# Kernel tuning notes

Measured on AMD Instinct MI355X. Metric: run time of the kernel, lower is better.

## Reference

```python
import jax, jax.numpy as jnp
import numpy as np

B, T, E = 8, 2048, 1024  # batch, seq_len, emb_size (= output_emb_size)


def setup_inputs() -> dict:
    key = jax.random.key(0)
    k1, k2, k3, k4, k5, k6, k7 = jax.random.split(key, 7)
    return {
        "q": jax.random.normal(k1, (B, T, E), jnp.float32),
        "k": jax.random.normal(k2, (B, T, E), jnp.float32),
        "v": jax.random.normal(k3, (B, T, E), jnp.float32),
        "mask": jax.random.randint(k4, (T, T), 0, 2, jnp.int32),
        # nn.Linear weights, stored [out, in] as in torch; applied as x @ W.T
        "Wq": jax.random.normal(k5, (E, E), jnp.float32) / np.sqrt(E),
        "Wk": jax.random.normal(k6, (E, E), jnp.float32) / np.sqrt(E),
        "Wv": jax.random.normal(k7, (E, E), jnp.float32) / np.sqrt(E),
    }


def reference(q, k, v, mask, Wq, Wk, Wv):
    # QKV projections (bias-free Linear): x @ W.T
    query = jnp.einsum("bte,oe->bto", q, Wq)
    key_p = jnp.einsum("bse,oe->bso", k, Wk)
    value = jnp.einsum("bse,oe->bso", v, Wv)
    d = key_p.shape[-1]
    scores = jnp.einsum("bto,bso->bts", query, key_p) / np.sqrt(d).astype(jnp.float32)
    # torch.any(mask): mask is nonzero somewhere -> apply masked_fill(mask==0, -inf)
    scores = jnp.where(mask[None, :, :] == 0, -jnp.inf, scores)
    weights = jax.nn.softmax(scores, axis=-1)
    return jnp.einsum("bts,bso->bto", weights, value)
```

## Files before the change

### kernel.cpp

```cpp
#include <hip/hip_runtime.h>
#include <hip/hip_bf16.h>

typedef __attribute__((ext_vector_type(8))) short short8;
typedef __attribute__((ext_vector_type(8))) unsigned short ushortx8;
typedef __attribute__((ext_vector_type(4))) unsigned short ushortx4;
typedef __attribute__((ext_vector_type(4))) float floatx4;

#define NB 8
#define NT 2048
#define NE 1024

__device__ __forceinline__ unsigned short f2bf(float f){
  unsigned int u = __builtin_bit_cast(unsigned int, f);
  u += 0x7FFFu + ((u >> 16) & 1u);
  return (unsigned short)(u >> 16);
}
__device__ __forceinline__ float bf2f(unsigned short h){
  unsigned int u = ((unsigned int)h) << 16;
  return __builtin_bit_cast(float, u);
}

__device__ __forceinline__ void async16(void* lds, const void* g){
  __builtin_amdgcn_global_load_lds(
      (const __attribute__((address_space(1))) unsigned int*)g,
      (__attribute__((address_space(3))) unsigned int*)lds, 16, 0, 0);
}

__global__ __launch_bounds__(256) void cvt3(const float* __restrict__ a0,
                                            const float* __restrict__ a1,
                                            const float* __restrict__ a2,
                                            unsigned short* __restrict__ out,
                                            int n4_per){
  const float* src = blockIdx.y == 0 ? a0 : (blockIdx.y == 1 ? a1 : a2);
  unsigned short* dst = out + (size_t)blockIdx.y * (size_t)n4_per * 4;
  int i = blockIdx.x * 256 + threadIdx.x;
  if (i < n4_per){
    floatx4 f = ((const floatx4*)src)[i];
    ushortx4 o;
    o.x = f2bf(f.x); o.y = f2bf(f.y); o.z = f2bf(f.z); o.w = f2bf(f.w);
    *(ushortx4*)(dst + (size_t)i * 4) = o;
  }
}

__global__ __launch_bounds__(256) void pack_mask(const int* __restrict__ m,
                                                 unsigned long long* __restrict__ bits){
  int t = blockIdx.x * 256 + threadIdx.x;
  const int4* p = (const int4*)(m + (size_t)t * 64);
  unsigned long long w = 0;
  #pragma unroll
  for (int jj = 0; jj < 16; jj++){
    int4 v = p[jj];
    w |= (unsigned long long)(v.x != 0) << (jj * 4 + 0);
    w |= (unsigned long long)(v.y != 0) << (jj * 4 + 1);
    w |= (unsigned long long)(v.z != 0) << (jj * 4 + 2);
    w |= (unsigned long long)(v.w != 0) << (jj * 4 + 3);
  }
  bits[t] = w;
}

template<int EPI>
__global__ __launch_bounds__(256) void gemm_nt(
    const unsigned short* __restrict__ A, long strideA,
    const unsigned short* __restrict__ B, long strideB,
    void* __restrict__ Out, long strideOutBytes,
    const unsigned long long* __restrict__ mbits,
    int K, int gx, int gy)
{
  __shared__ __attribute__((aligned(16))) unsigned short As[128 * 64];
  __shared__ __attribute__((aligned(16))) unsigned short Bs[128 * 64];
  const int tid = threadIdx.x;
  const int lane = tid & 63, wave = tid >> 6;

  int L = blockIdx.x;
  int xcd = L & 7, t = L >> 3;
  int x = t % gx;
  int strip = xcd + ((t / gx) << 3);
  int y = strip % gy, z = strip / gy;
  const int m0 = y << 7, n0 = x << 7;
  const int Nn = gx << 7;

  const unsigned short* Az = A + (size_t)z * strideA;
  const unsigned short* Bz = B + (size_t)z * strideB;

  const char* gA[4]; const char* gB[4]; int lo[4];
  {
    int s0 = (wave << 8) + lane;
    #pragma unroll
    for (int i = 0; i < 4; i++){
      int s = s0 + (i << 6);
      int row = s >> 3;
      int c = (s & 7) ^ (row & 7);
      lo[i] = s << 4;
      gA[i] = (const char*)(Az + (size_t)(m0 + row) * K) + (c << 4);
      gB[i] = (const char*)(Bz + (size_t)(n0 + row) * K) + (c << 4);
    }
  }
  char* AsB = (char*)As;
  char* BsB = (char*)Bs;

  const int lm = lane & 15, qd = lane >> 4;
  const int wr = (wave >> 1) << 6, wc = (wave & 1) << 6;
  const int sw = lm & 7;
  const char* aB0 = AsB + (wr + lm) * 128 + ((qd ^ sw) << 4);
  const char* aB1 = AsB + (wr + lm) * 128 + (((4 + qd) ^ sw) << 4);
  const char* bB0 = BsB + (wc + lm) * 128 + ((qd ^ sw) << 4);
  const char* bB1 = BsB + (wc + lm) * 128 + (((4 + qd) ^ sw) << 4);

  floatx4 acc[4][4];
  floatx4 zero4 = {0.f, 0.f, 0.f, 0.f};
  #pragma unroll
  for (int a = 0; a < 4; a++)
    #pragma unroll
    for (int b = 0; b < 4; b++) acc[a][b] = zero4;

  for (int kk = 0; kk < K; kk += 64){
    #pragma unroll
    for (int i = 0; i < 4; i++){
      async16(AsB + lo[i], gA[i]);
      async16(BsB + lo[i], gB[i]);
      gA[i] += 128; gB[i] += 128;
    }
    __syncthreads();

    short8 a0[4], a1[4], b0[4], b1[4];
    #pragma unroll
    for (int mi = 0; mi < 4; mi++){
      a0[mi] = *(const short8*)(aB0 + mi * 2048);
      a1[mi] = *(const short8*)(aB1 + mi * 2048);
    }
    #pragma unroll
    for (int ni = 0; ni < 4; ni++){
      b0[ni] = *(const short8*)(bB0 + ni * 2048);
      b1[ni] = *(const short8*)(bB1 + ni * 2048);
    }
    #pragma unroll
    for (int mi = 0; mi < 4; mi++)
      #pragma unroll
      for (int ni = 0; ni < 4; ni++)
        acc[mi][ni] = __builtin_amdgcn_mfma_f32_16x16x32_bf16(a0[mi], b0[ni], acc[mi][ni], 0, 0, 0);
    #pragma unroll
    for (int mi = 0; mi < 4; mi++)
      #pragma unroll
      for (int ni = 0; ni < 4; ni++)
        acc[mi][ni] = __builtin_amdgcn_mfma_f32_16x16x32_bf16(a1[mi], b1[ni], acc[mi][ni], 0, 0, 0);
    __syncthreads();
  }

  char* OutZ = (char*)Out + (size_t)z * strideOutBytes;
  if constexpr (EPI == 1){
    int wcol = (n0 + wc) >> 6;
    #pragma unroll
    for (int mi = 0; mi < 4; mi++){
      #pragma unroll
      for (int i = 0; i < 4; i++){
        int row = m0 + wr + mi * 16 + qd * 4 + i;
        unsigned long long w = mbits[(size_t)row * (NT / 64) + wcol];
        unsigned short* po = (unsigned short*)OutZ + (size_t)row * Nn + n0 + wc;
        #pragma unroll
        for (int ni = 0; ni < 4; ni++){
          float vv = acc[mi][ni][i];
          float s = ((w >> (ni * 16 + lm)) & 1ull) ? vv * 0.03125f : -INFINITY;
          po[ni * 16 + lm] = f2bf(s);
        }
      }
    }
  } else {
    #pragma unroll
    for (int mi = 0; mi < 4; mi++){
      #pragma unroll
      for (int i = 0; i < 4; i++){
        int row = m0 + wr + mi * 16 + qd * 4 + i;
        #pragma unroll
        for (int ni = 0; ni < 4; ni++){
          int col = n0 + wc + ni * 16 + lm;
          float vv = acc[mi][ni][i];
          if constexpr (EPI == 0)
            ((unsigned short*)OutZ)[(size_t)row * Nn + col] = f2bf(vv);
          else
            ((float*)OutZ)[(size_t)row * Nn + col] = vv;
        }
      }
    }
  }
}

__global__ __launch_bounds__(256) void transpose_bf16(const unsigned short* __restrict__ in,
                                                      unsigned short* __restrict__ out,
                                                      int rows, int cols){
  __shared__ __attribute__((aligned(16))) unsigned short tile[64][72];
  const unsigned short* ib = in + (size_t)blockIdx.z * rows * cols;
  unsigned short* ob = out + (size_t)blockIdx.z * rows * cols;
  int r0 = blockIdx.x * 64;
  int c0 = blockIdx.y * 64;
  int tid = threadIdx.x;
  #pragma unroll
  for (int i = 0; i < 2; i++){
    int id = tid + i * 256;
    int r = id >> 3, c = (id & 7) * 8;
    ushortx8 v = *(const ushortx8*)(ib + (size_t)(r0 + r) * cols + c0 + c);
    *(ushortx8*)&tile[r][c] = v;
  }
  __syncthreads();
  #pragma unroll
  for (int i = 0; i < 2; i++){
    int id = tid + i * 256;
    int r = id >> 3, c = (id & 7) * 8;
    ushortx8 v;
    #pragma unroll
    for (int j = 0; j < 8; j++) v[j] = tile[c + j][r];
    *(ushortx8*)(ob + (size_t)(c0 + r) * rows + r0 + c) = v;
  }
}

__global__ __launch_bounds__(256) void softmax_rows(unsigned short* __restrict__ S){
  size_t row = blockIdx.x;
  unsigned short* p = S + row * NT;
  int tid = threadIdx.x;
  ushortx8 v = *(const ushortx8*)(p + tid * 8);
  float f[8];
  #pragma unroll
  for (int j = 0; j < 8; j++) f[j] = bf2f(v[j]);
  float mx = f[0];
  #pragma unroll
  for (int j = 1; j < 8; j++) mx = fmaxf(mx, f[j]);
  #pragma unroll
  for (int off = 32; off > 0; off >>= 1) mx = fmaxf(mx, __shfl_xor(mx, off, 64));
  __shared__ float redm[4], reds[4];
  int lane = tid & 63, wv = tid >> 6;
  if (lane == 0) redm[wv] = mx;
  __syncthreads();
  mx = fmaxf(fmaxf(redm[0], redm[1]), fmaxf(redm[2], redm[3]));
  float e[8]; float se = 0.f;
  #pragma unroll
  for (int j = 0; j < 8; j++){ e[j] = __expf(f[j] - mx); se += e[j]; }
  #pragma unroll
  for (int off = 32; off > 0; off >>= 1) se += __shfl_xor(se, off, 64);
  if (lane == 0) reds[wv] = se;
  __syncthreads();
  se = reds[0] + reds[1] + reds[2] + reds[3];
  float inv = 1.f / se;
  ushortx8 o;
  #pragma unroll
  for (int j = 0; j < 8; j++) o[j] = f2bf(e[j] * inv);
  *(ushortx8*)(p + tid * 8) = o;
}

extern "C" void kernel_launch(void* const* d_in, const int* in_sizes, int n_in,
                              void* d_out, int out_size, void* d_ws, size_t ws_size,
                              hipStream_t stream){
  const float* q  = (const float*)d_in[0];
  const float* k  = (const float*)d_in[1];
  const float* v  = (const float*)d_in[2];
  const int* mask = (const int*)d_in[3];
  const float* Wq = (const float*)d_in[4];
  const float* Wk = (const float*)d_in[5];
  const float* Wv = (const float*)d_in[6];

  const size_t BTE = (size_t)NB * NT * NE;
  unsigned short* ws   = (unsigned short*)d_ws;
  unsigned short* QKVp = ws;
  unsigned short* VpT  = ws + 3 * BTE;
  unsigned short* Sb   = ws + 3 * BTE + BTE;
  unsigned short* Qin  = ws + 3 * BTE;
  unsigned short* Wb   = ws + 3 * BTE + BTE + (size_t)NB * NT * NT;
  unsigned long long* mbits = (unsigned long long*)(Wb + (size_t)3 * NE * NE);

  unsigned short* Qp = QKVp;
  unsigned short* Kp = QKVp + BTE;
  unsigned short* Vp = QKVp + 2 * BTE;

  cvt3<<<dim3(16384, 3), 256, 0, stream>>>(q, k, v, Qin, (int)(BTE / 4));
  cvt3<<<dim3(1024, 3), 256, 0, stream>>>(Wq, Wk, Wv, Wb, NE * NE / 4);
  pack_mask<<<256, 256, 0, stream>>>(mask, mbits);

  gemm_nt<0><<<3072, 256, 0, stream>>>(
      Qin, (long)BTE, Wb, (long)NE * NE,
      QKVp, (long)BTE * 2, nullptr, NE, 8, 128);

  transpose_bf16<<<dim3(32, 16, 8), 256, 0, stream>>>(Vp, VpT, NT, NE);

  gemm_nt<1><<<2048, 256, 0, stream>>>(
      Qp, (long)NT * NE, Kp, (long)NT * NE,
      Sb, (long)NT * NT * 2, mbits, NE, 16, 16);

  softmax_rows<<<dim3(NB * NT), 256, 0, stream>>>(Sb);

  gemm_nt<2><<<1024, 256, 0, stream>>>(
      Sb, (long)NT * NT, VpT, (long)NE * NT,
      d_out, (long)NT * NE * 4, nullptr, NT, 8, 16);
}
```

Before: 544.0 us.

## Fuse softmax into score GEMM epilogue and V transpose into projection epilogue

The score GEMM epilogue now computes exp(score/32) directly, with masked entries set to zero, and atomically accumulates per-row sums. The final GEMM divides by those sums, which removes the separate softmax pass over the B*T*T score matrix. The V projection writes its output transposed through LDS, so the standalone transpose kernel is gone. The softmax drops max-subtraction, which risks overflow for large scores, and the atomics add contention and make the row sums nondeterministic.

Measured after the change: 547.6 us. About the same (+0.7%).

```diff
diff --git a/kernel.cpp b/kernel.cpp
--- a/kernel.cpp
+++ b/kernel.cpp
@@ -58,16 +58,23 @@
   bits[t] = w;
 }
 
+__global__ __launch_bounds__(256) void zero_rs(float* __restrict__ p){
+  p[blockIdx.x * 256 + threadIdx.x] = 0.0f;
+}
+
 template<int EPI>
 __global__ __launch_bounds__(256) void gemm_nt(
     const unsigned short* __restrict__ A, long strideA,
     const unsigned short* __restrict__ B, long strideB,
     void* __restrict__ Out, long strideOutBytes,
     const unsigned long long* __restrict__ mbits,
+    float* __restrict__ rowsum,
     int K, int gx, int gy)
 {
-  __shared__ __attribute__((aligned(16))) unsigned short As[128 * 64];
-  __shared__ __attribute__((aligned(16))) unsigned short Bs[128 * 64];
+  constexpr int SMEM_SHORTS = (EPI == 0) ? 17408 : 16384;
+  __shared__ __attribute__((aligned(16))) unsigned short smem[SMEM_SHORTS];
+  unsigned short* As = smem;
+  unsigned short* Bs = smem + 8192;
   const int tid = threadIdx.x;
   const int lane = tid & 63, wave = tid >> 6;
 
@@ -147,7 +154,38 @@
   }
 
   char* OutZ = (char*)Out + (size_t)z * strideOutBytes;
-  if constexpr (EPI == 1){
+  if constexpr (EPI == 0){
+    if (z < 2){
+      #pragma unroll
+      for (int mi = 0; mi < 4; mi++)
+        #pragma unroll
+        for (int i = 0; i < 4; i++){
+          int row = m0 + wr + mi * 16 + qd * 4 + i;
+          #pragma unroll
+          for (int ni = 0; ni < 4; ni++)
+            ((unsigned short*)OutZ)[(size_t)row * Nn + wc + n0 + ni * 16 + lm] =
+                f2bf(acc[mi][ni][i]);
+        }
+    } else {
+      #pragma unroll
+      for (int mi = 0; mi < 4; mi++)
+        #pragma unroll
+        for (int ni = 0; ni < 4; ni++)
+          #pragma unroll
+          for (int i = 0; i < 4; i++)
+            smem[(wc + ni * 16 + lm) * 136 + (wr + mi * 16 + qd * 4 + i)] =
+                f2bf(acc[mi][ni][i]);
+      __syncthreads();
+      int c = tid >> 1, half = tid & 1;
+      int b = m0 >> 11;
+      unsigned short* dst = (unsigned short*)OutZ + (size_t)b * NE * NT +
+                            (size_t)(n0 + c) * NT + (m0 & 2047) + half * 64;
+      const unsigned short* srcp = smem + c * 136 + half * 64;
+      #pragma unroll
+      for (int j = 0; j < 8; j++)
+        *(ushortx8*)(dst + j * 8) = *(const ushortx8*)(srcp + j * 8);
+    }
+  } else if constexpr (EPI == 1){
     int wcol = (n0 + wc) >> 6;
     #pragma unroll
     for (int mi = 0; mi < 4; mi++){
@@ -156,12 +194,20 @@
         int row = m0 + wr + mi * 16 + qd * 4 + i;
         unsigned long long w = mbits[(size_t)row * (NT / 64) + wcol];
         unsigned short* po = (unsigned short*)OutZ + (size_t)row * Nn + n0 + wc;
+        float partial = 0.0f;
         #pragma unroll
         for (int ni = 0; ni < 4; ni++){
-          float vv = acc[mi][ni][i];
-          float s = ((w >> (ni * 16 + lm)) & 1ull) ? vv * 0.03125f : -INFINITY;
-          po[ni * 16 + lm] = f2bf(s);
+          float p = ((w >> (ni * 16 + lm)) & 1ull)
+                        ? __expf(acc[mi][ni][i] * 0.03125f) : 0.0f;
+          unsigned short h = f2bf(p);
+          partial += bf2f(h);
+          po[ni * 16 + lm] = h;
         }
+        partial += __shfl_xor(partial, 1, 64);
+        partial += __shfl_xor(partial, 2, 64);
+        partial += __shfl_xor(partial, 4, 64);
+        partial += __shfl_xor(partial, 8, 64);
+        if (lm == 0) atomicAdd(&rowsum[(size_t)z * NT + row], partial);
       }
     }
   } else {
@@ -170,79 +216,14 @@
       #pragma unroll
       for (int i = 0; i < 4; i++){
         int row = m0 + wr + mi * 16 + qd * 4 + i;
-        #pragma unroll
-        for (int ni = 0; ni < 4; ni++){
-          int col = n0 + wc + ni * 16 + lm;
-          float vv = acc[mi][ni][i];
-          if constexpr (EPI == 0)
-            ((unsigned short*)OutZ)[(size_t)row * Nn + col] = f2bf(vv);
-          else
-            ((float*)OutZ)[(size_t)row * Nn + col] = vv;
-        }
+        float inv = 1.0f / rowsum[(size_t)z * NT + row];
+        #pragma unroll
+        for (int ni = 0; ni < 4; ni++)
+          ((float*)OutZ)[(size_t)row * Nn + n0 + wc + ni * 16 + lm] =
+              acc[mi][ni][i] * inv;
       }
     }
   }
-}
-
-__global__ __launch_bounds__(256) void transpose_bf16(const unsigned short* __restrict__ in,
-                                                      unsigned short* __restrict__ out,
-                                                      int rows, int cols){
-  __shared__ __attribute__((aligned(16))) unsigned short tile[64][72];
-  const unsigned short* ib = in + (size_t)blockIdx.z * rows * cols;
-  unsigned short* ob = out + (size_t)blockIdx.z * rows * cols;
-  int r0 = blockIdx.x * 64;
-  int c0 = blockIdx.y * 64;
-  int tid = threadIdx.x;
-  #pragma unroll
-  for (int i = 0; i < 2; i++){
-    int id = tid + i * 256;
-    int r = id >> 3, c = (id & 7) * 8;
-    ushortx8 v = *(const ushortx8*)(ib + (size_t)(r0 + r) * cols + c0 + c);
-    *(ushortx8*)&tile[r][c] = v;
-  }
-  __syncthreads();
-  #pragma unroll
-  for (int i = 0; i < 2; i++){
-    int id = tid + i * 256;
-    int r = id >> 3, c = (id & 7) * 8;
-    ushortx8 v;
-    #pragma unroll
-    for (int j = 0; j < 8; j++) v[j] = tile[c + j][r];
-    *(ushortx8*)(ob + (size_t)(c0 + r) * rows + r0 + c) = v;
-  }
-}
-
-__global__ __launch_bounds__(256) void softmax_rows(unsigned short* __restrict__ S){
-  size_t row = blockIdx.x;
-  unsigned short* p = S + row * NT;
-  int tid = threadIdx.x;
-  ushortx8 v = *(const ushortx8*)(p + tid * 8);
-  float f[8];
-  #pragma unroll
-  for (int j = 0; j < 8; j++) f[j] = bf2f(v[j]);
-  float mx = f[0];
-  #pragma unroll
-  for (int j = 1; j < 8; j++) mx = fmaxf(mx, f[j]);
-  #pragma unroll
-  for (int off = 32; off > 0; off >>= 1) mx = fmaxf(mx, __shfl_xor(mx, off, 64));
-  __shared__ float redm[4], reds[4];
-  int lane = tid & 63, wv = tid >> 6;
-  if (lane == 0) redm[wv] = mx;
-  __syncthreads();
-  mx = fmaxf(fmaxf(redm[0], redm[1]), fmaxf(redm[2], redm[3]));
-  float e[8]; float se = 0.f;
-  #pragma unroll
-  for (int j = 0; j < 8; j++){ e[j] = __expf(f[j] - mx); se += e[j]; }
-  #pragma unroll
-  for (int off = 32; off > 0; off >>= 1) se += __shfl_xor(se, off, 64);
-  if (lane == 0) reds[wv] = se;
-  __syncthreads();
-  se = reds[0] + reds[1] + reds[2] + reds[3];
-  float inv = 1.f / se;
-  ushortx8 o;
-  #pragma unroll
-  for (int j = 0; j < 8; j++) o[j] = f2bf(e[j] * inv);
-  *(ushortx8*)(p + tid * 8) = o;
 }
 
 extern "C" void kernel_launch(void* const* d_in, const int* in_sizes, int n_in,
@@ -259,33 +240,29 @@
   const size_t BTE = (size_t)NB * NT * NE;
   unsigned short* ws   = (unsigned short*)d_ws;
   unsigned short* QKVp = ws;
-  unsigned short* VpT  = ws + 3 * BTE;
-  unsigned short* Sb   = ws + 3 * BTE + BTE;
+  unsigned short* Qp   = QKVp;
+  unsigned short* Kp   = QKVp + BTE;
+  unsigned short* VpT  = QKVp + 2 * BTE;
   unsigned short* Qin  = ws + 3 * BTE;
-  unsigned short* Wb   = ws + 3 * BTE + BTE + (size_t)NB * NT * NT;
+  unsigned short* Sb   = ws + 3 * BTE;
+  unsigned short* Wb   = ws + 6 * BTE;
   unsigned long long* mbits = (unsigned long long*)(Wb + (size_t)3 * NE * NE);
-
-  unsigned short* Qp = QKVp;
-  unsigned short* Kp = QKVp + BTE;
-  unsigned short* Vp = QKVp + 2 * BTE;
+  float* rowsum = (float*)(mbits + (size_t)NT * NT / 64);
 
   cvt3<<<dim3(16384, 3), 256, 0, stream>>>(q, k, v, Qin, (int)(BTE / 4));
   cvt3<<<dim3(1024, 3), 256, 0, stream>>>(Wq, Wk, Wv, Wb, NE * NE / 4);
   pack_mask<<<256, 256, 0, stream>>>(mask, mbits);
+  zero_rs<<<NB * NT / 256, 256, 0, stream>>>(rowsum);
 
   gemm_nt<0><<<3072, 256, 0, stream>>>(
       Qin, (long)BTE, Wb, (long)NE * NE,
-      QKVp, (long)BTE * 2, nullptr, NE, 8, 128);
-
-  transpose_bf16<<<dim3(32, 16, 8), 256, 0, stream>>>(Vp, VpT, NT, NE);
+      QKVp, (long)BTE * 2, nullptr, nullptr, NE, 8, 128);
 
   gemm_nt<1><<<2048, 256, 0, stream>>>(
       Qp, (long)NT * NE, Kp, (long)NT * NE,
-      Sb, (long)NT * NT * 2, mbits, NE, 16, 16);
-
-  softmax_rows<<<dim3(NB * NT), 256, 0, stream>>>(Sb);
+      Sb, (long)NT * NT * 2, mbits, rowsum, NE, 16, 16);
 
   gemm_nt<2><<<1024, 256, 0, stream>>>(
       Sb, (long)NT * NT, VpT, (long)NE * NT,
-      d_out, (long)NT * NE * 4, nullptr, NT, 8, 16);
-}
+      d_out, (long)NT * NE * 4, nullptr, rowsum, NT, 8, 16);
+}
```
